# Optimization experiments

Hardware: AMD Instinct MI355X
Metric: run time of the kernel (lower is better)

Reference implementation:

```python
import jax, jax.numpy as jnp
import numpy as np

B, N, T, F_IN = 256, 300, 64, 3
U0_DIM, U1_DIM = 256, 256
F_OUT = 2
W_SCALE = 0.03  # small init so the relu recurrence stays bounded


def setup_inputs() -> dict:
    key = jax.random.key(0)
    ks = jax.random.split(key, 9)
    f32 = jnp.float32
    return {
        "x":  jax.random.normal(ks[0], (B, N, T, F_IN), f32),
        "W0": jax.random.normal(ks[1], (N * F_IN, 4 * U0_DIM), f32) * W_SCALE,
        "U0": jax.random.normal(ks[2], (U0_DIM, 4 * U0_DIM), f32) * W_SCALE,
        "b0": jnp.zeros((4 * U0_DIM,), f32),
        "W1": jax.random.normal(ks[3], (U0_DIM, 4 * U1_DIM), f32) * W_SCALE,
        "U1": jax.random.normal(ks[4], (U1_DIM, 4 * U1_DIM), f32) * W_SCALE,
        "b1": jnp.zeros((4 * U1_DIM,), f32),
        "Wd": jax.random.normal(ks[5], (U1_DIM, N * F_OUT), f32) * W_SCALE,
        "bd": jnp.zeros((N * F_OUT,), f32),
    }


def _lstm(seq, W, U, b):
    """Keras LSTM with activation='relu', recurrent_activation='sigmoid'.
    seq: (B, T, D) -> (B, T, units). Gate order: i, f, g(c), o."""
    units = U.shape[0]
    # precompute input contribution for all timesteps: (B, T, 4U)
    zx = jnp.einsum('btd,dg->btg', seq, W) + b

    def step(carry, zt):
        h, c = carry
        z = zt + h @ U                         # (B, 4U)
        i, f, g, o = jnp.split(z, 4, axis=-1)
        i = jax.nn.sigmoid(i)
        f = jax.nn.sigmoid(f)
        g = jax.nn.relu(g)                     # activation='relu'
        o = jax.nn.sigmoid(o)
        c = f * c + i * g
        h = o * jax.nn.relu(c)                 # activation='relu' on cell
        return (h, c), h

    h0 = jnp.zeros((seq.shape[0], units), seq.dtype)
    (_, _), hs = jax.lax.scan(step, (h0, h0), jnp.swapaxes(zx, 0, 1))
    return jnp.swapaxes(hs, 0, 1)              # (B, T, units)


def reference(x, W0, U0, b0, W1, U1, b1, Wd, bd):
    Bn, Nn, Tn, Fi = x.shape
    out = jnp.transpose(x, (0, 2, 1, 3)).reshape(Bn, Tn, Nn * Fi)  # (B,T,N*F)
    out = _lstm(out, W0, U0, b0)
    out = _lstm(out, W1, U1, b1)
    out = out @ Wd + bd                                            # (B,T,N*F_OUT)
    out = out.reshape(Bn, Tn, Nn, -1)
    return jnp.transpose(out, (0, 2, 1, 3))                        # (B,N,T,F_OUT)
```

## Files before the change

kernel.cpp:

```cpp
#include <hip/hip_runtime.h>
#include <hip/hip_bf16.h>
#include <hip/hip_fp16.h>


typedef _Float16 half8 __attribute__((ext_vector_type(8)));
typedef float floatx4 __attribute__((ext_vector_type(4)));

#define B_SZ   256
#define T_STEPS 64
#define N_SEQ  300
#define M_ROWS 16384
#define K0P    928
#define G4     1024
#define UD     256
#define NOUT   600
#define NOUTP  640

#define OFF_MODE   ((size_t)0)
#define OFF_FLAGS  ((size_t)256)
#define OFF_BIAS   ((size_t)512)
#define OFF_XT     ((size_t)16384)
#define SZ_XT      ((size_t)M_ROWS * K0P * 2)
#define OFF_W0T    (OFF_XT + SZ_XT)
#define SZ_W0T     ((size_t)G4 * K0P * 2)
#define OFF_U0T    (OFF_W0T + SZ_W0T)
#define SZ_UT      ((size_t)G4 * UD * 2)
#define OFF_W1T    (OFF_U0T + SZ_UT)
#define OFF_U1T    (OFF_W1T + SZ_UT)
#define OFF_WDT    (OFF_U1T + SZ_UT)
#define SZ_WDT     ((size_t)NOUTP * UD * 2)
#define OFF_HBUF   (OFF_WDT + SZ_WDT)
#define SZ_HBUF    ((size_t)16 * 2 * 2 * 4096)
#define OFF_ZX0    (OFF_HBUF + SZ_HBUF)
#define SZ_ZX      ((size_t)M_ROWS * G4 * 2)
#define OFF_H0     (OFF_ZX0 + SZ_ZX)
#define SZ_H       ((size_t)M_ROWS * UD * 2)
#define OFF_ZX1    (OFF_H0 + SZ_H)
#define OFF_H1     (OFF_ZX1 + SZ_ZX)
#define WS_NEEDED  (OFF_H1 + SZ_H)

__device__ __forceinline__ float load_in(const void* p, size_t idx, int mode) {
  if (mode) {
    unsigned v = ((const unsigned short*)p)[idx];
    return __uint_as_float(v << 16);
  }
  return ((const float*)p)[idx];
}

__global__ void sniff_init(const unsigned* __restrict__ x, int* __restrict__ modeflag,
                           unsigned* __restrict__ flags) {
  __shared__ int cnt;
  if (threadIdx.x == 0) cnt = 0;
  __syncthreads();
  unsigned w = x[threadIdx.x];
  unsigned e = (w >> 8) & 0x7fu;
  if (e >= 0x3au && e <= 0x42u) atomicAdd(&cnt, 1);
  __syncthreads();
  if (threadIdx.x == 0) *modeflag = (cnt >= 128) ? 1 : 0;
  if (threadIdx.x < 64) flags[threadIdx.x] = 0u;
}

__global__ void cvt_bias(const void* __restrict__ b0, const void* __restrict__ b1,
                         const void* __restrict__ bd, float* __restrict__ outb,
                         const int* __restrict__ modeflag) {
  int mode = *modeflag;
  int i = blockIdx.x * 256 + threadIdx.x;
  if (i < 1024)       outb[i] = load_in(b0, i, mode);
  else if (i < 2048)  outb[i] = load_in(b1, i - 1024, mode);
  else if (i < 2648)  outb[i] = load_in(bd, i - 2048, mode);
}

__global__ void transpose_cast(const void* __restrict__ in, _Float16* __restrict__ out,
                               int Rin, int Cin, int Nout, int Kout,
                               const int* __restrict__ modeflag) {
  int mode = *modeflag;
  __shared__ float tile[32][33];
  int k0 = blockIdx.x * 32, n0 = blockIdx.y * 32;
  int tx = threadIdx.x, ty = threadIdx.y;
  #pragma unroll
  for (int i = 0; i < 32; i += 8) {
    int k = k0 + ty + i, n = n0 + tx;
    tile[ty + i][tx] = (k < Rin && n < Cin) ? load_in(in, (size_t)k * Cin + n, mode) : 0.f;
  }
  __syncthreads();
  #pragma unroll
  for (int i = 0; i < 32; i += 8) {
    int n = n0 + ty + i, k = k0 + tx;
    if (n < Nout && k < Kout)
      out[(size_t)n * Kout + k] = (_Float16)tile[tx][ty + i];
  }
}

__global__ void transpose_x(const void* __restrict__ x, _Float16* __restrict__ xt,
                            const int* __restrict__ modeflag) {
  int mode = *modeflag;
  int b = blockIdx.y, ch = blockIdx.x;
  __shared__ _Float16 tile[60 * 192];
  int n0 = ch * 60;
  size_t basein = ((size_t)b * N_SEQ + n0) * 192;
  for (int i = threadIdx.x; i < 60 * 192; i += 256)
    tile[i] = (_Float16)load_in(x, basein + i, mode);
  __syncthreads();
  for (int i = threadIdx.x; i < 64 * 180; i += 256) {
    int t = i / 180, cz = i % 180;
    int nn = cz / 3, f = cz % 3;
    xt[((size_t)b * 64 + t) * K0P + n0 * 3 + cz] = tile[nn * 192 + t * 3 + f];
  }
  if (ch == 4) {
    for (int i = threadIdx.x; i < 64 * 28; i += 256) {
      int t = i / 28, z = i % 28;
      xt[((size_t)b * 64 + t) * K0P + 900 + z] = (_Float16)0.f;
    }
  }
}

template <int OUT_MODE>
__global__ __launch_bounds__(256)
void gemm_f16(const _Float16* __restrict__ A, const _Float16* __restrict__ BT,
              const float* __restrict__ bias, void* __restrict__ Cout,
              int N, int K, int Nreal, const int* __restrict__ modeflag) {
  __shared__ _Float16 As[128 * 40];
  __shared__ _Float16 Bs[128 * 40];
  int tid = threadIdx.x;
  int wv = tid >> 6, lane = tid & 63;
  int q = lane >> 4, l15 = lane & 15;
  int wm = wv >> 1, wn = wv & 1;
  int row0 = blockIdx.y * 128, col0 = blockIdx.x * 128;
  floatx4 acc[4][4] = {};
  int r_st = tid >> 1;
  int c_st = (tid & 1) * 2;
  const _Float16* Arow = A + (size_t)(row0 + r_st) * K + c_st * 8;
  const _Float16* Brow = BT + (size_t)(col0 + r_st) * K + c_st * 8;
  _Float16* AsW = As + r_st * 40 + c_st * 8;
  _Float16* BsW = Bs + r_st * 40 + c_st * 8;

  for (int k0 = 0; k0 < K; k0 += 32) {
    __syncthreads();
    half8 a0 = *(const half8*)(Arow + k0);
    half8 a1 = *(const half8*)(Arow + k0 + 8);
    half8 b0v = *(const half8*)(Brow + k0);
    half8 b1v = *(const half8*)(Brow + k0 + 8);
    *(half8*)(AsW) = a0;  *(half8*)(AsW + 8) = a1;
    *(half8*)(BsW) = b0v; *(half8*)(BsW + 8) = b1v;
    __syncthreads();
    half8 af[4], bf[4];
    #pragma unroll
    for (int i = 0; i < 4; ++i)
      af[i] = *(const half8*)(As + (wm * 64 + i * 16 + l15) * 40 + q * 8);
    #pragma unroll
    for (int j = 0; j < 4; ++j)
      bf[j] = *(const half8*)(Bs + (wn * 64 + j * 16 + l15) * 40 + q * 8);
    #pragma unroll
    for (int i = 0; i < 4; ++i)
      #pragma unroll
      for (int j = 0; j < 4; ++j)
        acc[i][j] = __builtin_amdgcn_mfma_f32_16x16x32_f16(af[i], bf[j], acc[i][j], 0, 0, 0);
  }

  int mode = 0;
  if (OUT_MODE == 1) mode = *modeflag;
  #pragma unroll
  for (int j = 0; j < 4; ++j) {
    int col = col0 + wn * 64 + j * 16 + l15;
    float bv = (col < Nreal) ? bias[col] : 0.f;
    #pragma unroll
    for (int i = 0; i < 4; ++i) {
      int rowb = row0 + wm * 64 + i * 16 + q * 4;
      #pragma unroll
      for (int r = 0; r < 4; ++r) {
        float v = acc[i][j][r] + bv;
        int row = rowb + r;
        if (OUT_MODE == 0) {
          ((_Float16*)Cout)[(size_t)row * N + col] = (_Float16)v;
        } else {
          if (col < Nreal) {
            size_t idx = (size_t)(row >> 6) * 38400 + (size_t)(col >> 1) * 128
                       + (size_t)(row & 63) * 2 + (col & 1);
            if (mode) ((__hip_bfloat16*)Cout)[idx] = __float2bfloat16(v);
            else      ((float*)Cout)[idx] = v;
          }
        }
      }
    }
  }
}

__global__ __launch_bounds__(512, 2)
void lstm_rec(const _Float16* __restrict__ zx, const _Float16* __restrict__ UT,
              _Float16* __restrict__ hseq, unsigned long long* __restrict__ pay,
              unsigned* __restrict__ flags) {
  int tid = threadIdx.x;
  int wv = tid >> 6, lane = tid & 63;
  int q = lane >> 4, l15 = lane & 15;
  int c = blockIdx.x >> 4;
  int g = blockIdx.x & 15;
  int ubase = c * 128 + wv * 16;
  int ucol = ubase + l15;

  __shared__ _Float16 hlds[2][16 * 128];

  half8 uf[4][8];
  #pragma unroll
  for (int G = 0; G < 4; ++G) {
    const _Float16* Urow = UT + (size_t)(G * 256 + ucol) * UD;
    #pragma unroll
    for (int s = 0; s < 8; ++s)
      uf[G][s] = *(const half8*)(Urow + s * 32 + q * 8);
  }
  half8 hf[8];
  #pragma unroll
  for (int s = 0; s < 8; ++s) hf[s] = (half8)(_Float16)0.f;
  floatx4 cst = {0.f, 0.f, 0.f, 0.f};

  unsigned* myflag = &flags[g * 2 + c];
  unsigned* pflag  = &flags[g * 2 + (1 - c)];
  unsigned long long* mypay = pay + (size_t)(g * 2 + c) * 1024;
  const unsigned long long* ppay = pay + (size_t)(g * 2 + (1 - c)) * 1024;

  int row = q * 4 + (lane & 3);
  int cq  = l15 & 12;
  int payi  = row * 32 + ((wv * 16 + cq) >> 2);
  int ldswb = (row * 256 + (wv * 16 + cq) * 2) ^ ((row & 7) << 4);
  unsigned long long* hsp =
      (unsigned long long*)(hseq + ((size_t)(g * 16 + row) * 64) * UD + ubase + cq);
  const _Float16* zb = zx + (size_t)(g * 16 + q * 4) * 64 * G4 + ucol;

  unsigned short zpre[16];
  #pragma unroll
  for (int G = 0; G < 4; ++G)
    #pragma unroll
    for (int r = 0; r < 4; ++r)
      zpre[G * 4 + r] = *(const unsigned short*)(zb + r * (64 * G4) + G * 256);

  for (int t = 0; t < 64; ++t) {
    floatx4 accv[4] = {};
    if (c == 0) {
      #pragma unroll
      for (int s = 0; s < 8; ++s) {
        accv[0] = __builtin_amdgcn_mfma_f32_16x16x32_f16(hf[s], uf[0][s], accv[0], 0, 0, 0);
        accv[1] = __builtin_amdgcn_mfma_f32_16x16x32_f16(hf[s], uf[1][s], accv[1], 0, 0, 0);
        accv[2] = __builtin_amdgcn_mfma_f32_16x16x32_f16(hf[s], uf[2][s], accv[2], 0, 0, 0);
        accv[3] = __builtin_amdgcn_mfma_f32_16x16x32_f16(hf[s], uf[3][s], accv[3], 0, 0, 0);
      }
    } else {
      #pragma unroll
      for (int ss = 0; ss < 8; ++ss) {
        int s = (ss + 4) & 7;
        accv[0] = __builtin_amdgcn_mfma_f32_16x16x32_f16(hf[s], uf[0][s], accv[0], 0, 0, 0);
        accv[1] = __builtin_amdgcn_mfma_f32_16x16x32_f16(hf[s], uf[1][s], accv[1], 0, 0, 0);
        accv[2] = __builtin_amdgcn_mfma_f32_16x16x32_f16(hf[s], uf[2][s], accv[2], 0, 0, 0);
        accv[3] = __builtin_amdgcn_mfma_f32_16x16x32_f16(hf[s], uf[3][s], accv[3], 0, 0, 0);
      }
    }

    _Float16 hh[4];
    #pragma unroll
    for (int r = 0; r < 4; ++r) {
      float zi = accv[0][r] + (float)__builtin_bit_cast(_Float16, zpre[0 + r]);
      float zf = accv[1][r] + (float)__builtin_bit_cast(_Float16, zpre[4 + r]);
      float zg = accv[2][r] + (float)__builtin_bit_cast(_Float16, zpre[8 + r]);
      float zo = accv[3][r] + (float)__builtin_bit_cast(_Float16, zpre[12 + r]);
      float ig = 1.f / (1.f + __expf(-zi));
      float fg = 1.f / (1.f + __expf(-zf));
      float gg = zg > 0.f ? zg : 0.f;
      float og = 1.f / (1.f + __expf(-zo));
      float cn = fg * cst[r] + ig * gg;
      cst[r] = cn;
      hh[r] = (_Float16)(og * (cn > 0.f ? cn : 0.f));
    }

    unsigned A  = ((unsigned)__builtin_bit_cast(unsigned short, hh[1]) << 16)
                |  (unsigned)__builtin_bit_cast(unsigned short, hh[0]);
    unsigned Bq = ((unsigned)__builtin_bit_cast(unsigned short, hh[3]) << 16)
                |  (unsigned)__builtin_bit_cast(unsigned short, hh[2]);
    unsigned T  = __shfl_xor((lane & 2) ? A : Bq, 2, 64);
    unsigned X0 = (lane & 2) ? T : A;
    unsigned X1 = (lane & 2) ? Bq : T;
    unsigned W  = (X0 & 0xffffu) | (X1 << 16);
    unsigned X  = (X0 >> 16) | (X1 & 0xffff0000u);
    unsigned R  = __shfl_xor((lane & 1) ? W : X, 1, 64);
    unsigned lo, hi;
    if (lane & 1) { lo = (R & 0xffffu) | (X << 16); hi = (R >> 16) | (X & 0xffff0000u); }
    else          { lo = (W & 0xffffu) | (R << 16); hi = (W >> 16) | (R & 0xffff0000u); }
    unsigned long long hp = ((unsigned long long)hi << 32) | lo;

    hsp[(size_t)t * 64] = hp;

    if (t < 63) {
      int par = t & 1;
      __hip_atomic_store(mypay + par * 512 + payi, hp, __ATOMIC_RELAXED,
                         __HIP_MEMORY_SCOPE_AGENT);
      *(unsigned long long*)((char*)hlds + par * 4096 + ldswb) = hp;
      #pragma unroll
      for (int G = 0; G < 4; ++G)
        #pragma unroll
        for (int r = 0; r < 4; ++r)
          zpre[G * 4 + r] =
              *(const unsigned short*)(zb + r * (64 * G4) + (t + 1) * G4 + G * 256);
      __syncthreads();
      if (tid == 0)
        __hip_atomic_store(myflag, (unsigned)(t + 1), __ATOMIC_RELAXED,
                           __HIP_MEMORY_SCOPE_AGENT);
      while (__hip_atomic_load(pflag, __ATOMIC_RELAXED, __HIP_MEMORY_SCOPE_AGENT)
             <= (unsigned)t)
        __builtin_amdgcn_s_sleep(1);
      asm volatile("" ::: "memory");
      const unsigned long long* pp = ppay + par * 512;
      if (c == 0) {
        #pragma unroll
        for (int sl = 0; sl < 4; ++sl) {
          union { unsigned long long u[2]; half8 v; } cv;
          cv.u[0] = __hip_atomic_load(pp + (l15 * 32 + sl * 8 + q * 2),
                                      __ATOMIC_RELAXED, __HIP_MEMORY_SCOPE_AGENT);
          cv.u[1] = __hip_atomic_load(pp + (l15 * 32 + sl * 8 + q * 2 + 1),
                                      __ATOMIC_RELAXED, __HIP_MEMORY_SCOPE_AGENT);
          hf[4 + sl] = cv.v;
        }
        #pragma unroll
        for (int sl = 0; sl < 4; ++sl) {
          int rb = (l15 * 256 + sl * 64 + q * 16) ^ ((l15 & 7) << 4);
          hf[sl] = *(const half8*)((const char*)hlds + par * 4096 + rb);
        }
      } else {
        #pragma unroll
        for (int sl = 0; sl < 4; ++sl) {
          union { unsigned long long u[2]; half8 v; } cv;
          cv.u[0] = __hip_atomic_load(pp + (l15 * 32 + sl * 8 + q * 2),
                                      __ATOMIC_RELAXED, __HIP_MEMORY_SCOPE_AGENT);
          cv.u[1] = __hip_atomic_load(pp + (l15 * 32 + sl * 8 + q * 2 + 1),
                                      __ATOMIC_RELAXED, __HIP_MEMORY_SCOPE_AGENT);
          hf[sl] = cv.v;
        }
        #pragma unroll
        for (int sl = 0; sl < 4; ++sl) {
          int rb = (l15 * 256 + sl * 64 + q * 16) ^ ((l15 & 7) << 4);
          hf[4 + sl] = *(const half8*)((const char*)hlds + par * 4096 + rb);
        }
      }
    }
  }
}

extern "C" void kernel_launch(void* const* d_in, const int* in_sizes, int n_in,
                              void* d_out, int out_size, void* d_ws, size_t ws_size,
                              hipStream_t stream) {
  if (ws_size < WS_NEEDED) return;

  const void* x  = d_in[0];
  const void* W0 = d_in[1];
  const void* U0 = d_in[2];
  const void* b0 = d_in[3];
  const void* W1 = d_in[4];
  const void* U1 = d_in[5];
  const void* b1 = d_in[6];
  const void* Wd = d_in[7];
  const void* bd = d_in[8];

  char* ws = (char*)d_ws;
  int*       mf    = (int*)(ws + OFF_MODE);
  unsigned*  flags = (unsigned*)(ws + OFF_FLAGS);
  float*     biasf = (float*)(ws + OFF_BIAS);
  _Float16*  xt    = (_Float16*)(ws + OFF_XT);
  _Float16*  W0T   = (_Float16*)(ws + OFF_W0T);
  _Float16*  U0T   = (_Float16*)(ws + OFF_U0T);
  _Float16*  W1T   = (_Float16*)(ws + OFF_W1T);
  _Float16*  U1T   = (_Float16*)(ws + OFF_U1T);
  _Float16*  WdT   = (_Float16*)(ws + OFF_WDT);
  unsigned long long* pay = (unsigned long long*)(ws + OFF_HBUF);
  _Float16*  zx0   = (_Float16*)(ws + OFF_ZX0);
  _Float16*  h0    = (_Float16*)(ws + OFF_H0);
  _Float16*  zx1   = (_Float16*)(ws + OFF_ZX1);
  _Float16*  h1    = (_Float16*)(ws + OFF_H1);

  sniff_init<<<1, 256, 0, stream>>>((const unsigned*)x, mf, flags);
  cvt_bias<<<11, 256, 0, stream>>>(b0, b1, bd, biasf, mf);

  transpose_cast<<<dim3(K0P / 32, G4 / 32), dim3(32, 8), 0, stream>>>(W0, W0T, 900, 1024, 1024, K0P, mf);
  transpose_cast<<<dim3(UD / 32, G4 / 32), dim3(32, 8), 0, stream>>>(U0, U0T, 256, 1024, 1024, UD, mf);
  transpose_cast<<<dim3(UD / 32, G4 / 32), dim3(32, 8), 0, stream>>>(W1, W1T, 256, 1024, 1024, UD, mf);
  transpose_cast<<<dim3(UD / 32, G4 / 32), dim3(32, 8), 0, stream>>>(U1, U1T, 256, 1024, 1024, UD, mf);
  transpose_cast<<<dim3(UD / 32, NOUTP / 32), dim3(32, 8), 0, stream>>>(Wd, WdT, 256, 600, NOUTP, UD, mf);

  transpose_x<<<dim3(5, B_SZ), 256, 0, stream>>>(x, xt, mf);

  gemm_f16<0><<<dim3(G4 / 128, M_ROWS / 128), 256, 0, stream>>>(xt, W0T, biasf, zx0, G4, K0P, G4, mf);
  lstm_rec<<<32, 512, 0, stream>>>(zx0, U0T, h0, pay, flags);
  gemm_f16<0><<<dim3(G4 / 128, M_ROWS / 128), 256, 0, stream>>>(h0, W1T, biasf + 1024, zx1, G4, UD, G4, mf);
  lstm_rec<<<32, 512, 0, stream>>>(zx1, U1T, h1, pay, flags + 32);
  gemm_f16<1><<<dim3(NOUTP / 128, M_ROWS / 128), 256, 0, stream>>>(h1, WdT, biasf + 2048, d_out, NOUTP, UD, NOUT, mf);
}
```

Baseline: 748.8 us.

## Replace flag handshake with per-timestep sentinel-polled payload buffers in LSTM recurrence

The separate flag store plus flag spin-wait is replaced by a per-timestep payload buffer pre-filled with a NaN sentinel. Consumers poll the payload words directly until none equal the sentinel. This removes one cross-block round trip per step and the write-after-read hazard of the double buffer. A fill kernel runs before each recurrence, which adds memory traffic, and the second layer reuses the zx0 buffer to shrink the workspace. If a real h value ever produced that exact NaN bit pattern, the poll would never exit.

```diff
diff --git a/kernel.cpp b/kernel.cpp
--- a/kernel.cpp
+++ b/kernel.cpp
@@ -16,9 +16,11 @@
 #define NOUT   600
 #define NOUTP  640
 
+#define HSENT  0x7E007E007E007E00ULL
+
 #define OFF_MODE   ((size_t)0)
 #define OFF_FLAGS  ((size_t)256)
-#define OFF_BIAS   ((size_t)512)
+#define OFF_BIAS   ((size_t)768)
 #define OFF_XT     ((size_t)16384)
 #define SZ_XT      ((size_t)M_ROWS * K0P * 2)
 #define OFF_W0T    (OFF_XT + SZ_XT)
@@ -30,13 +32,12 @@
 #define OFF_WDT    (OFF_U1T + SZ_UT)
 #define SZ_WDT     ((size_t)NOUTP * UD * 2)
 #define OFF_HBUF   (OFF_WDT + SZ_WDT)
-#define SZ_HBUF    ((size_t)16 * 2 * 2 * 4096)
+#define SZ_HBUF    ((size_t)16 * 2 * 64 * 512 * 8)
 #define OFF_ZX0    (OFF_HBUF + SZ_HBUF)
 #define SZ_ZX      ((size_t)M_ROWS * G4 * 2)
 #define OFF_H0     (OFF_ZX0 + SZ_ZX)
 #define SZ_H       ((size_t)M_ROWS * UD * 2)
-#define OFF_ZX1    (OFF_H0 + SZ_H)
-#define OFF_H1     (OFF_ZX1 + SZ_ZX)
+#define OFF_H1     (OFF_H0 + SZ_H)
 #define WS_NEEDED  (OFF_H1 + SZ_H)
 
 __device__ __forceinline__ float load_in(const void* p, size_t idx, int mode) {
@@ -57,7 +58,12 @@
   if (e >= 0x3au && e <= 0x42u) atomicAdd(&cnt, 1);
   __syncthreads();
   if (threadIdx.x == 0) *modeflag = (cnt >= 128) ? 1 : 0;
-  if (threadIdx.x < 64) flags[threadIdx.x] = 0u;
+  if (threadIdx.x < 128) flags[threadIdx.x] = 0u;
+}
+
+__global__ void fill_sentinel(unsigned long long* __restrict__ p) {
+  size_t i = (size_t)blockIdx.x * 256 + threadIdx.x;
+  p[i] = HSENT;
 }
 
 __global__ void cvt_bias(const void* __restrict__ b0, const void* __restrict__ b1,
@@ -187,8 +193,7 @@
 
 __global__ __launch_bounds__(512, 2)
 void lstm_rec(const _Float16* __restrict__ zx, const _Float16* __restrict__ UT,
-              _Float16* __restrict__ hseq, unsigned long long* __restrict__ pay,
-              unsigned* __restrict__ flags) {
+              _Float16* __restrict__ hseq, unsigned long long* __restrict__ pay) {
   int tid = threadIdx.x;
   int wv = tid >> 6, lane = tid & 63;
   int q = lane >> 4, l15 = lane & 15;
@@ -212,10 +217,8 @@
   for (int s = 0; s < 8; ++s) hf[s] = (half8)(_Float16)0.f;
   floatx4 cst = {0.f, 0.f, 0.f, 0.f};
 
-  unsigned* myflag = &flags[g * 2 + c];
-  unsigned* pflag  = &flags[g * 2 + (1 - c)];
-  unsigned long long* mypay = pay + (size_t)(g * 2 + c) * 1024;
-  const unsigned long long* ppay = pay + (size_t)(g * 2 + (1 - c)) * 1024;
+  unsigned long long* mypay = pay + (size_t)(g * 2 + c) * 64 * 512;
+  const unsigned long long* ppay = pay + (size_t)(g * 2 + (1 - c)) * 64 * 512;
 
   int row = q * 4 + (lane & 3);
   int cq  = l15 & 12;
@@ -288,7 +291,7 @@
 
     if (t < 63) {
       int par = t & 1;
-      __hip_atomic_store(mypay + par * 512 + payi, hp, __ATOMIC_RELAXED,
+      __hip_atomic_store(mypay + (size_t)t * 512 + payi, hp, __ATOMIC_RELAXED,
                          __HIP_MEMORY_SCOPE_AGENT);
       *(unsigned long long*)((char*)hlds + par * 4096 + ldswb) = hp;
       #pragma unroll
@@ -298,39 +301,36 @@
           zpre[G * 4 + r] =
               *(const unsigned short*)(zb + r * (64 * G4) + (t + 1) * G4 + G * 256);
       __syncthreads();
-      if (tid == 0)
-        __hip_atomic_store(myflag, (unsigned)(t + 1), __ATOMIC_RELAXED,
-                           __HIP_MEMORY_SCOPE_AGENT);
-      while (__hip_atomic_load(pflag, __ATOMIC_RELAXED, __HIP_MEMORY_SCOPE_AGENT)
-             <= (unsigned)t)
+
+      const unsigned long long* pp = ppay + (size_t)t * 512 + (l15 * 32 + q * 2);
+      unsigned long long v0, v1, v2, v3, v4, v5, v6, v7;
+      for (;;) {
+        v0 = __hip_atomic_load(pp + 0,  __ATOMIC_RELAXED, __HIP_MEMORY_SCOPE_AGENT);
+        v1 = __hip_atomic_load(pp + 1,  __ATOMIC_RELAXED, __HIP_MEMORY_SCOPE_AGENT);
+        v2 = __hip_atomic_load(pp + 8,  __ATOMIC_RELAXED, __HIP_MEMORY_SCOPE_AGENT);
+        v3 = __hip_atomic_load(pp + 9,  __ATOMIC_RELAXED, __HIP_MEMORY_SCOPE_AGENT);
+        v4 = __hip_atomic_load(pp + 16, __ATOMIC_RELAXED, __HIP_MEMORY_SCOPE_AGENT);
+        v5 = __hip_atomic_load(pp + 17, __ATOMIC_RELAXED, __HIP_MEMORY_SCOPE_AGENT);
+        v6 = __hip_atomic_load(pp + 24, __ATOMIC_RELAXED, __HIP_MEMORY_SCOPE_AGENT);
+        v7 = __hip_atomic_load(pp + 25, __ATOMIC_RELAXED, __HIP_MEMORY_SCOPE_AGENT);
+        if (v0 != HSENT && v1 != HSENT && v2 != HSENT && v3 != HSENT &&
+            v4 != HSENT && v5 != HSENT && v6 != HSENT && v7 != HSENT) break;
         __builtin_amdgcn_s_sleep(1);
-      asm volatile("" ::: "memory");
-      const unsigned long long* pp = ppay + par * 512;
+      }
+      union { unsigned long long u[2]; half8 v; } cv0, cv1, cv2, cv3;
+      cv0.u[0] = v0; cv0.u[1] = v1;
+      cv1.u[0] = v2; cv1.u[1] = v3;
+      cv2.u[0] = v4; cv2.u[1] = v5;
+      cv3.u[0] = v6; cv3.u[1] = v7;
       if (c == 0) {
-        #pragma unroll
-        for (int sl = 0; sl < 4; ++sl) {
-          union { unsigned long long u[2]; half8 v; } cv;
-          cv.u[0] = __hip_atomic_load(pp + (l15 * 32 + sl * 8 + q * 2),
-                                      __ATOMIC_RELAXED, __HIP_MEMORY_SCOPE_AGENT);
-          cv.u[1] = __hip_atomic_load(pp + (l15 * 32 + sl * 8 + q * 2 + 1),
-                                      __ATOMIC_RELAXED, __HIP_MEMORY_SCOPE_AGENT);
-          hf[4 + sl] = cv.v;
-        }
+        hf[4] = cv0.v; hf[5] = cv1.v; hf[6] = cv2.v; hf[7] = cv3.v;
         #pragma unroll
         for (int sl = 0; sl < 4; ++sl) {
           int rb = (l15 * 256 + sl * 64 + q * 16) ^ ((l15 & 7) << 4);
           hf[sl] = *(const half8*)((const char*)hlds + par * 4096 + rb);
         }
       } else {
-        #pragma unroll
-        for (int sl = 0; sl < 4; ++sl) {
-          union { unsigned long long u[2]; half8 v; } cv;
-          cv.u[0] = __hip_atomic_load(pp + (l15 * 32 + sl * 8 + q * 2),
-                                      __ATOMIC_RELAXED, __HIP_MEMORY_SCOPE_AGENT);
-          cv.u[1] = __hip_atomic_load(pp + (l15 * 32 + sl * 8 + q * 2 + 1),
-                                      __ATOMIC_RELAXED, __HIP_MEMORY_SCOPE_AGENT);
-          hf[sl] = cv.v;
-        }
+        hf[0] = cv0.v; hf[1] = cv1.v; hf[2] = cv2.v; hf[3] = cv3.v;
         #pragma unroll
         for (int sl = 0; sl < 4; ++sl) {
           int rb = (l15 * 256 + sl * 64 + q * 16) ^ ((l15 & 7) << 4);
@@ -369,7 +369,7 @@
   unsigned long long* pay = (unsigned long long*)(ws + OFF_HBUF);
   _Float16*  zx0   = (_Float16*)(ws + OFF_ZX0);
   _Float16*  h0    = (_Float16*)(ws + OFF_H0);
-  _Float16*  zx1   = (_Float16*)(ws + OFF_ZX1);
+  _Float16*  zx1   = (_Float16*)(ws + OFF_ZX0);
   _Float16*  h1    = (_Float16*)(ws + OFF_H1);
 
   sniff_init<<<1, 256, 0, stream>>>((const unsigned*)x, mf, flags);
@@ -382,10 +382,12 @@
   transpose_cast<<<dim3(UD / 32, NOUTP / 32), dim3(32, 8), 0, stream>>>(Wd, WdT, 256, 600, NOUTP, UD, mf);
 
   transpose_x<<<dim3(5, B_SZ), 256, 0, stream>>>(x, xt, mf);
+  fill_sentinel<<<4096, 256, 0, stream>>>(pay);
 
   gemm_f16<0><<<dim3(G4 / 128, M_ROWS / 128), 256, 0, stream>>>(xt, W0T, biasf, zx0, G4, K0P, G4, mf);
-  lstm_rec<<<32, 512, 0, stream>>>(zx0, U0T, h0, pay, flags);
+  lstm_rec<<<32, 512, 0, stream>>>(zx0, U0T, h0, pay);
+  fill_sentinel<<<4096, 256, 0, stream>>>(pay);
   gemm_f16<0><<<dim3(G4 / 128, M_ROWS / 128), 256, 0, stream>>>(h0, W1T, biasf + 1024, zx1, G4, UD, G4, mf);
-  lstm_rec<<<32, 512, 0, stream>>>(zx1, U1T, h1, pay, flags + 32);
+  lstm_rec<<<32, 512, 0, stream>>>(zx1, U1T, h1, pay);
   gemm_f16<1><<<dim3(NOUTP / 128, M_ROWS / 128), 256, 0, stream>>>(h1, WdT, biasf + 2048, d_out, NOUTP, UD, NOUT, mf);
 }
```

Measured after the change: 747.5 us. No clear change (-0.2%).
